# Kernel optimization log

Measured on AMD Instinct MI355X. Metric: run time of the kernel, lower is better.

Reference implementation:

```python
import jax, jax.numpy as jnp
import numpy as np

EPS_SINKHORN = 0.01   # entropic regularization (cost / eps)
EPS_LOG = 1e-8        # numerical epsilon inside logs
NUM_ITERS = 50


def setup_inputs() -> dict:
    key = jax.random.key(0)
    k1, k2 = jax.random.split(key)
    B, N = 8, 2048
    x1 = jax.random.normal(k1, (B, N, 3), dtype=jnp.float32)
    x2 = jax.random.normal(k2, (B, N, 3), dtype=jnp.float32)
    return {"x1": x1, "x2": x2}


def reference(x1, x2):
    # x1, x2: [B, N, 3] point clouds
    B, N, _ = x1.shape
    # pairwise squared-distance cost matrix: [B, N, N]
    cost = jnp.sum((x1[:, :, None, :] - x2[:, None, :, :]) ** 2, axis=-1)
    K = jnp.exp(-cost / EPS_SINKHORN)  # constant across iterations

    inv_n = jnp.float32(1.0 / N)
    mu = jnp.full((B, N), inv_n, dtype=cost.dtype)
    nu = jnp.full((B, N), inv_n, dtype=cost.dtype)
    log_mu = jnp.log(mu + EPS_LOG)
    log_nu = jnp.log(nu + EPS_LOG)

    def step(carry, _):
        u, v = carry
        # row update: sum_j K_ij * exp(v_j)
        u = log_mu - jnp.log(jnp.einsum('bij,bj->bi', K, jnp.exp(v)) + EPS_LOG)
        # col update: sum_i K_ij * exp(u_i)
        v = log_nu - jnp.log(jnp.einsum('bij,bi->bj', K, jnp.exp(u)) + EPS_LOG)
        return (u, v), None

    u0 = jnp.zeros((B, N), dtype=cost.dtype)
    v0 = jnp.zeros((B, N), dtype=cost.dtype)
    (u, v), _ = jax.lax.scan(step, (u0, v0), None, length=NUM_ITERS)

    transport = K * jnp.exp(u[:, :, None] + v[:, None, :])  # [B, N, N]
    emd = jnp.sum(transport * cost, axis=(1, 2))            # [B]
    return emd
```

## Files before the change

kernel.cpp:

```cpp
#include <hip/hip_runtime.h>
#include <cmath>

#define BATCH 8
#define NPT   2048
#define NPAIR (NPT / 2)
#define NPTS  (BATCH * NPT)
#define TILES 64
#define GRID_MAIN (BATCH * TILES)
#define THREADS 512
#define RPW   4
#define ITERS 50

#define C_LOG2E 1.4426950408889634f
#define NEG100C (-144.26950408889634f)
#define S200C   288.53900817779268f
#define EPS_LOG 1e-8f
#define LN2_01  0.006931471805599453f

typedef float v2f __attribute__((ext_vector_type(2)));
typedef float v4f __attribute__((ext_vector_type(4)));
typedef unsigned long long u64t;

static __device__ __forceinline__ float fast_exp2(float x) {
#if __has_builtin(__builtin_amdgcn_exp2f)
    return __builtin_amdgcn_exp2f(x);
#else
    return exp2f(x);
#endif
}

static __device__ __forceinline__ v2f pk_fma(v2f a, v2f b, v2f c) {
    v2f d;
    asm("v_pk_fma_f32 %0, %1, %2, %3" : "=v"(d) : "v"(a), "v"(b), "v"(c));
    return d;
}
static __device__ __forceinline__ v2f pk_add(v2f a, v2f b) {
    v2f d;
    asm("v_pk_add_f32 %0, %1, %2" : "=v"(d) : "v"(a), "v"(b));
    return d;
}

static __device__ __forceinline__ float gload(const float* p) {
    return __hip_atomic_load(p, __ATOMIC_RELAXED, __HIP_MEMORY_SCOPE_AGENT);
}
static __device__ __forceinline__ void gstore(float* p, float val) {
    __hip_atomic_store(p, val, __ATOMIC_RELAXED, __HIP_MEMORY_SCOPE_AGENT);
}
static __device__ __forceinline__ u64t gload2(const float* p) {
    return __hip_atomic_load((const u64t*)p, __ATOMIC_RELAXED,
                             __HIP_MEMORY_SCOPE_AGENT);
}

__global__ void init_kernel(float* __restrict__ out,
                            unsigned int* __restrict__ flags) {
    int t = threadIdx.x;
    if (t < BATCH) out[t] = 0.0f;
    flags[t] = 0u;
}

static __device__ __forceinline__ void flag_barrier(unsigned int* bflags,
                                                    int tile, int wave,
                                                    int lane,
                                                    unsigned int phase) {
    __syncthreads();
    if (wave == 0) {
        if (lane == 0)
            __hip_atomic_store(&bflags[tile], phase, __ATOMIC_RELAXED,
                               __HIP_MEMORY_SCOPE_AGENT);
        while (__hip_atomic_load(&bflags[lane], __ATOMIC_RELAXED,
                                 __HIP_MEMORY_SCOPE_AGENT) < phase) {
            __builtin_amdgcn_s_sleep(1);
        }
    }
    __syncthreads();
    __builtin_amdgcn_sched_barrier(0);
}

static __device__ __forceinline__ void fold_dual(v4f* cdZW, const float* dual,
        int base, int tid, const float (&Pa)[2], const float (&Pb)[2]) {
    u64t d0 = gload2(dual + base + 4 * tid);
    u64t d1 = gload2(dual + base + 4 * tid + 2);
    float a0 = __uint_as_float((unsigned)d0);
    float b0 = __uint_as_float((unsigned)(d0 >> 32));
    float a1 = __uint_as_float((unsigned)d1);
    float b1 = __uint_as_float((unsigned)(d1 >> 32));
    reinterpret_cast<v2f*>(&cdZW[2 * tid])[1] =
        (v2f){fmaf(C_LOG2E, a0, Pa[0]), fmaf(C_LOG2E, b0, Pb[0])};
    reinterpret_cast<v2f*>(&cdZW[2 * tid + 1])[1] =
        (v2f){fmaf(C_LOG2E, a1, Pa[1]), fmaf(C_LOG2E, b1, Pb[1])};
}

static __device__ __forceinline__ void half_pass(
        const v4f* cdXY, const v4f* cdZW,
        const v2f (&rx)[RPW], const v2f (&ry)[RPW],
        const v2f (&rz)[RPW], const v2f (&rc)[RPW],
        float* __restrict__ dual_out, int outbase, int lane, float log_mu)
{
    v2f acc[RPW];
#pragma unroll
    for (int r = 0; r < RPW; r++) acc[r] = (v2f){0.0f, 0.0f};

#pragma unroll 2
    for (int jp = 0; jp < NPAIR; jp += 64) {
        v4f a  = cdXY[jp + lane];
        v4f bz = cdZW[jp + lane];
        v2f xx = __builtin_shufflevector(a,  a,  0, 1);
        v2f yy = __builtin_shufflevector(a,  a,  2, 3);
        v2f zz = __builtin_shufflevector(bz, bz, 0, 1);
        v2f ww = __builtin_shufflevector(bz, bz, 2, 3);
#pragma unroll
        for (int r = 0; r < RPW; r++) {
            v2f t = pk_fma(xx, rx[r], ww);
            t = pk_fma(yy, ry[r], t);
            t = pk_fma(zz, rz[r], t);
            t = pk_add(t, rc[r]);
            acc[r].x += fast_exp2(t.x);
            acc[r].y += fast_exp2(t.y);
        }
    }

    float sel = 1.0f;
#pragma unroll
    for (int r = 0; r < RPW; r++) {
        float s = acc[r].x + acc[r].y;
#pragma unroll
        for (int m = 32; m >= 1; m >>= 1) s += __shfl_xor(s, m, 64);
        if (lane == r) sel = s;
    }
    float res = log_mu - __logf(sel + EPS_LOG);
    if (lane < RPW) gstore(&dual_out[outbase + lane], res);
}

__global__ __launch_bounds__(THREADS, 4) void sinkhorn_kernel(
        const float* __restrict__ x1, const float* __restrict__ x2,
        float* __restrict__ u, float* __restrict__ v,
        unsigned int* __restrict__ flags, float* __restrict__ out)
{
    __shared__ v4f cd1XY[NPAIR], cd1ZW[NPAIR];
    __shared__ v4f cd2XY[NPAIR], cd2ZW[NPAIR];

    const int b    = blockIdx.x / TILES;
    const int tile = blockIdx.x % TILES;
    const int base = b * NPT;
    unsigned int* bflags = flags + b * TILES;

    const int tid  = threadIdx.x;
    const int wave = tid >> 6;
    const int lane = tid & 63;
    const int row0 = tile * 32 + wave * RPW;

    const float log_mu = logf(1.0f / (float)NPT + EPS_LOG);

    float P1a[2], P1b[2], P2a[2], P2b[2];
#pragma unroll
    for (int k = 0; k < 2; k++) {
        int q = 2 * tid + k;
        const float* p = x1 + 3 * (base + 2 * q);
        float ax = p[0], ay = p[1], az = p[2];
        float bx = p[3], by = p[4], bz = p[5];
        float na = fmaf(ax, ax, fmaf(ay, ay, az * az));
        float nb = fmaf(bx, bx, fmaf(by, by, bz * bz));
        P1a[k] = na * NEG100C;  P1b[k] = nb * NEG100C;
        cd1XY[q] = (v4f){ax * S200C, bx * S200C, ay * S200C, by * S200C};
        cd1ZW[q] = (v4f){az * S200C, bz * S200C, P1a[k], P1b[k]};

        p = x2 + 3 * (base + 2 * q);
        ax = p[0]; ay = p[1]; az = p[2];
        bx = p[3]; by = p[4]; bz = p[5];
        na = fmaf(ax, ax, fmaf(ay, ay, az * az));
        nb = fmaf(bx, bx, fmaf(by, by, bz * bz));
        P2a[k] = na * NEG100C;  P2b[k] = nb * NEG100C;
        cd2XY[q] = (v4f){ax * S200C, bx * S200C, ay * S200C, by * S200C};
        cd2ZW[q] = (v4f){az * S200C, bz * S200C, P2a[k], P2b[k]};
    }

    v2f rx1[RPW], ry1[RPW], rz1[RPW], rc1[RPW];
    v2f rx2[RPW], ry2[RPW], rz2[RPW], rc2[RPW];
    float rc1s[RPW];
#pragma unroll
    for (int r = 0; r < RPW; r++) {
        const float* p = x1 + 3 * (base + row0 + r);
        float a = p[0], bb = p[1], c = p[2];
        float nn = NEG100C * fmaf(a, a, fmaf(bb, bb, c * c));
        rx1[r] = (v2f){a, a};  ry1[r] = (v2f){bb, bb};
        rz1[r] = (v2f){c, c};  rc1[r] = (v2f){nn, nn};
        rc1s[r] = nn;
        p = x2 + 3 * (base + row0 + r);
        a = p[0]; bb = p[1]; c = p[2];
        nn = NEG100C * fmaf(a, a, fmaf(bb, bb, c * c));
        rx2[r] = (v2f){a, a};  ry2[r] = (v2f){bb, bb};
        rz2[r] = (v2f){c, c};  rc2[r] = (v2f){nn, nn};
    }
    __syncthreads();

    unsigned int phase = 0;
    for (int it = 0; it < ITERS; it++) {
        if (it > 0) {
            fold_dual(cd2ZW, v, base, tid, P2a, P2b);
            __syncthreads();
        }
        half_pass(cd2XY, cd2ZW, rx1, ry1, rz1, rc1, u, base + row0, lane, log_mu);
        flag_barrier(bflags, tile, wave, lane, ++phase);

        fold_dual(cd1ZW, u, base, tid, P1a, P1b);
        __syncthreads();
        half_pass(cd1XY, cd1ZW, rx2, ry2, rz2, rc2, v, base + row0, lane, log_mu);
        flag_barrier(bflags, tile, wave, lane, ++phase);
    }

    v2f* cvp = reinterpret_cast<v2f*>(cd1XY);
    {
        u64t d0 = gload2(v + base + 4 * tid);
        u64t d1 = gload2(v + base + 4 * tid + 2);
        float a0 = __uint_as_float((unsigned)d0);
        float b0 = __uint_as_float((unsigned)(d0 >> 32));
        float a1 = __uint_as_float((unsigned)d1);
        float b1 = __uint_as_float((unsigned)(d1 >> 32));
        reinterpret_cast<v2f*>(&cd2ZW[2 * tid])[1] =
            (v2f){fmaf(C_LOG2E, a0, P2a[0]), fmaf(C_LOG2E, b0, P2b[0])};
        reinterpret_cast<v2f*>(&cd2ZW[2 * tid + 1])[1] =
            (v2f){fmaf(C_LOG2E, a1, P2a[1]), fmaf(C_LOG2E, b1, P2b[1])};
        cvp[2 * tid]     = (v2f){0.01f * a0, 0.01f * b0};
        cvp[2 * tid + 1] = (v2f){0.01f * a1, 0.01f * b1};
    }
    __syncthreads();

    v2f rcc[RPW], su[RPW];
#pragma unroll
    for (int r = 0; r < RPW; r++) {
        float ur  = gload(&u[base + row0 + r]);
        float rcs = fmaf(C_LOG2E, ur, rc1s[r]);
        rcc[r] = (v2f){rcs, rcs};
        float sus = 0.01f * ur;
        su[r] = (v2f){sus, sus};
    }

    const v2f NL2 = {-LN2_01, -LN2_01};
    v2f eacc = {0.0f, 0.0f};
#pragma unroll 2
    for (int jp = 0; jp < NPAIR; jp += 64) {
        v4f a   = cd2XY[jp + lane];
        v4f bz  = cd2ZW[jp + lane];
        v2f cv2 = cvp[jp + lane];
        v2f xx = __builtin_shufflevector(a,  a,  0, 1);
        v2f yy = __builtin_shufflevector(a,  a,  2, 3);
        v2f zz = __builtin_shufflevector(bz, bz, 0, 1);
        v2f ww = __builtin_shufflevector(bz, bz, 2, 3);
#pragma unroll
        for (int r = 0; r < RPW; r++) {
            v2f t = pk_fma(xx, rx1[r], ww);
            t = pk_fma(yy, ry1[r], t);
            t = pk_fma(zz, rz1[r], t);
            t = pk_add(t, rcc[r]);
            v2f c2 = pk_fma(t, NL2, pk_add(su[r], cv2));
            eacc.x = fmaf(fast_exp2(t.x), c2.x, eacc.x);
            eacc.y = fmaf(fast_exp2(t.y), c2.y, eacc.y);
        }
    }
    float es = eacc.x + eacc.y;
#pragma unroll
    for (int m = 32; m >= 1; m >>= 1) es += __shfl_xor(es, m, 64);

    float* wsum = reinterpret_cast<float*>(cd2XY);
    if (lane == 0) wsum[wave] = es;
    __syncthreads();
    if (tid == 0) {
        float s = 0.0f;
#pragma unroll
        for (int w = 0; w < THREADS / 64; w++) s += wsum[w];
        atomicAdd(&out[b], s);
    }
}

extern "C" void kernel_launch(void* const* d_in, const int* in_sizes, int n_in,
                              void* d_out, int out_size, void* d_ws, size_t ws_size,
                              hipStream_t stream) {
    (void)in_sizes; (void)n_in; (void)out_size; (void)ws_size;
    const float* x1 = (const float*)d_in[0];
    const float* x2 = (const float*)d_in[1];
    float* out = (float*)d_out;

    char* ws = (char*)d_ws;
    float* u = (float*)ws;
    float* v = u + NPTS;
    unsigned int* flags = (unsigned int*)(v + NPTS);

    init_kernel<<<1, 512, 0, stream>>>(out, flags);
    sinkhorn_kernel<<<GRID_MAIN, THREADS, 0, stream>>>(x1, x2, u, v, flags, out);
}
```

Baseline: 843.2 us.

## Process two batches per block with split arrive/wait barriers over 256 blocks

Each block now handles the same row tile for two batches (b and b+4) with 1024 threads and 2 rows per wave, shrinking the grid to 256 blocks. The grid barrier is split into an arrive step and a wait step, so the second batch's half-pass runs before the block waits on the first batch's flags. The dual fold is merged into the loop body and the last iteration skips the v fold. The intent is to hide barrier latency and fit the persistent grid on the available CUs, at the cost of larger LDS use per block and fewer rows per wave to amortize each shared-memory load.

```diff
diff --git a/kernel.cpp b/kernel.cpp
--- a/kernel.cpp
+++ b/kernel.cpp
@@ -6,9 +6,9 @@
 #define NPAIR (NPT / 2)
 #define NPTS  (BATCH * NPT)
 #define TILES 64
-#define GRID_MAIN (BATCH * TILES)
-#define THREADS 512
-#define RPW   4
+#define GRID_MAIN 256
+#define THREADS 1024
+#define RPW   2
 #define ITERS 50
 
 #define C_LOG2E 1.4426950408889634f
@@ -58,36 +58,24 @@
     flags[t] = 0u;
 }
 
-static __device__ __forceinline__ void flag_barrier(unsigned int* bflags,
-                                                    int tile, int wave,
-                                                    int lane,
-                                                    unsigned int phase) {
-    __syncthreads();
+static __device__ __forceinline__ void bar_arrive(unsigned int* flags,
+                                                  int slot, unsigned int ph) {
+    __syncthreads();
+    if (threadIdx.x == 0)
+        __hip_atomic_store(&flags[slot], ph, __ATOMIC_RELAXED,
+                           __HIP_MEMORY_SCOPE_AGENT);
+}
+static __device__ __forceinline__ void bar_wait(const unsigned int* bflags,
+                                                int wave, int lane,
+                                                unsigned int ph) {
     if (wave == 0) {
-        if (lane == 0)
-            __hip_atomic_store(&bflags[tile], phase, __ATOMIC_RELAXED,
-                               __HIP_MEMORY_SCOPE_AGENT);
         while (__hip_atomic_load(&bflags[lane], __ATOMIC_RELAXED,
-                                 __HIP_MEMORY_SCOPE_AGENT) < phase) {
+                                 __HIP_MEMORY_SCOPE_AGENT) < ph) {
             __builtin_amdgcn_s_sleep(1);
         }
     }
     __syncthreads();
     __builtin_amdgcn_sched_barrier(0);
-}
-
-static __device__ __forceinline__ void fold_dual(v4f* cdZW, const float* dual,
-        int base, int tid, const float (&Pa)[2], const float (&Pb)[2]) {
-    u64t d0 = gload2(dual + base + 4 * tid);
-    u64t d1 = gload2(dual + base + 4 * tid + 2);
-    float a0 = __uint_as_float((unsigned)d0);
-    float b0 = __uint_as_float((unsigned)(d0 >> 32));
-    float a1 = __uint_as_float((unsigned)d1);
-    float b1 = __uint_as_float((unsigned)(d1 >> 32));
-    reinterpret_cast<v2f*>(&cdZW[2 * tid])[1] =
-        (v2f){fmaf(C_LOG2E, a0, Pa[0]), fmaf(C_LOG2E, b0, Pb[0])};
-    reinterpret_cast<v2f*>(&cdZW[2 * tid + 1])[1] =
-        (v2f){fmaf(C_LOG2E, a1, Pa[1]), fmaf(C_LOG2E, b1, Pb[1])};
 }
 
 static __device__ __forceinline__ void half_pass(
@@ -136,13 +124,16 @@
         float* __restrict__ u, float* __restrict__ v,
         unsigned int* __restrict__ flags, float* __restrict__ out)
 {
-    __shared__ v4f cd1XY[NPAIR], cd1ZW[NPAIR];
-    __shared__ v4f cd2XY[NPAIR], cd2ZW[NPAIR];
-
-    const int b    = blockIdx.x / TILES;
+    __shared__ v4f c1XY[2][NPAIR], c1ZW[2][NPAIR];
+    __shared__ v4f c2XY[2][NPAIR], c2ZW[2][NPAIR];
+
+    const int b0   = blockIdx.x / TILES;
     const int tile = blockIdx.x % TILES;
-    const int base = b * NPT;
-    unsigned int* bflags = flags + b * TILES;
+    const int bA = b0, bB = b0 + 4;
+    const int baseA = bA * NPT, baseB = bB * NPT;
+    const int slotA = bA * TILES + tile, slotB = bB * TILES + tile;
+    const unsigned int* flA = flags + bA * TILES;
+    const unsigned int* flB = flags + bB * TILES;
 
     const int tid  = threadIdx.x;
     const int wave = tid >> 6;
@@ -153,122 +144,168 @@
 
     float P1a[2], P1b[2], P2a[2], P2b[2];
 #pragma unroll
-    for (int k = 0; k < 2; k++) {
-        int q = 2 * tid + k;
-        const float* p = x1 + 3 * (base + 2 * q);
+    for (int g = 0; g < 2; g++) {
+        int base = g ? baseB : baseA;
+        const float* p = x1 + 3 * (base + 2 * tid);
         float ax = p[0], ay = p[1], az = p[2];
         float bx = p[3], by = p[4], bz = p[5];
         float na = fmaf(ax, ax, fmaf(ay, ay, az * az));
         float nb = fmaf(bx, bx, fmaf(by, by, bz * bz));
-        P1a[k] = na * NEG100C;  P1b[k] = nb * NEG100C;
-        cd1XY[q] = (v4f){ax * S200C, bx * S200C, ay * S200C, by * S200C};
-        cd1ZW[q] = (v4f){az * S200C, bz * S200C, P1a[k], P1b[k]};
-
-        p = x2 + 3 * (base + 2 * q);
+        P1a[g] = na * NEG100C;  P1b[g] = nb * NEG100C;
+        c1XY[g][tid] = (v4f){ax * S200C, bx * S200C, ay * S200C, by * S200C};
+        c1ZW[g][tid] = (v4f){az * S200C, bz * S200C, P1a[g], P1b[g]};
+
+        p = x2 + 3 * (base + 2 * tid);
         ax = p[0]; ay = p[1]; az = p[2];
         bx = p[3]; by = p[4]; bz = p[5];
         na = fmaf(ax, ax, fmaf(ay, ay, az * az));
         nb = fmaf(bx, bx, fmaf(by, by, bz * bz));
-        P2a[k] = na * NEG100C;  P2b[k] = nb * NEG100C;
-        cd2XY[q] = (v4f){ax * S200C, bx * S200C, ay * S200C, by * S200C};
-        cd2ZW[q] = (v4f){az * S200C, bz * S200C, P2a[k], P2b[k]};
-    }
-
-    v2f rx1[RPW], ry1[RPW], rz1[RPW], rc1[RPW];
-    v2f rx2[RPW], ry2[RPW], rz2[RPW], rc2[RPW];
-    float rc1s[RPW];
-#pragma unroll
-    for (int r = 0; r < RPW; r++) {
-        const float* p = x1 + 3 * (base + row0 + r);
-        float a = p[0], bb = p[1], c = p[2];
-        float nn = NEG100C * fmaf(a, a, fmaf(bb, bb, c * c));
-        rx1[r] = (v2f){a, a};  ry1[r] = (v2f){bb, bb};
-        rz1[r] = (v2f){c, c};  rc1[r] = (v2f){nn, nn};
-        rc1s[r] = nn;
-        p = x2 + 3 * (base + row0 + r);
-        a = p[0]; bb = p[1]; c = p[2];
-        nn = NEG100C * fmaf(a, a, fmaf(bb, bb, c * c));
-        rx2[r] = (v2f){a, a};  ry2[r] = (v2f){bb, bb};
-        rz2[r] = (v2f){c, c};  rc2[r] = (v2f){nn, nn};
-    }
-    __syncthreads();
-
-    unsigned int phase = 0;
+        P2a[g] = na * NEG100C;  P2b[g] = nb * NEG100C;
+        c2XY[g][tid] = (v4f){ax * S200C, bx * S200C, ay * S200C, by * S200C};
+        c2ZW[g][tid] = (v4f){az * S200C, bz * S200C, P2a[g], P2b[g]};
+    }
+
+    v2f rx1[2][RPW], ry1[2][RPW], rz1[2][RPW], rc1[2][RPW];
+    v2f rx2[2][RPW], ry2[2][RPW], rz2[2][RPW], rc2[2][RPW];
+    float rc1s[2][RPW];
+#pragma unroll
+    for (int g = 0; g < 2; g++) {
+        int base = g ? baseB : baseA;
+#pragma unroll
+        for (int r = 0; r < RPW; r++) {
+            const float* p = x1 + 3 * (base + row0 + r);
+            float a = p[0], bb = p[1], c = p[2];
+            float nn = NEG100C * fmaf(a, a, fmaf(bb, bb, c * c));
+            rx1[g][r] = (v2f){a, a};  ry1[g][r] = (v2f){bb, bb};
+            rz1[g][r] = (v2f){c, c};  rc1[g][r] = (v2f){nn, nn};
+            rc1s[g][r] = nn;
+            p = x2 + 3 * (base + row0 + r);
+            a = p[0]; bb = p[1]; c = p[2];
+            nn = NEG100C * fmaf(a, a, fmaf(bb, bb, c * c));
+            rx2[g][r] = (v2f){a, a};  ry2[g][r] = (v2f){bb, bb};
+            rz2[g][r] = (v2f){c, c};  rc2[g][r] = (v2f){nn, nn};
+        }
+    }
+    __syncthreads();
+
+    unsigned int ph = 0;
     for (int it = 0; it < ITERS; it++) {
-        if (it > 0) {
-            fold_dual(cd2ZW, v, base, tid, P2a, P2b);
-            __syncthreads();
-        }
-        half_pass(cd2XY, cd2ZW, rx1, ry1, rz1, rc1, u, base + row0, lane, log_mu);
-        flag_barrier(bflags, tile, wave, lane, ++phase);
-
-        fold_dual(cd1ZW, u, base, tid, P1a, P1b);
+        half_pass(c2XY[0], c2ZW[0], rx1[0], ry1[0], rz1[0], rc1[0],
+                  u, baseA + row0, lane, log_mu);
+        bar_arrive(flags, slotA, ph + 1);
+        half_pass(c2XY[1], c2ZW[1], rx1[1], ry1[1], rz1[1], rc1[1],
+                  u, baseB + row0, lane, log_mu);
+        bar_arrive(flags, slotB, ph + 1);
+        bar_wait(flA, wave, lane, ph + 1);
+        bar_wait(flB, wave, lane, ph + 1);
+        {
+            u64t dA = gload2(u + baseA + 2 * tid);
+            u64t dB = gload2(u + baseB + 2 * tid);
+            float aA = __uint_as_float((unsigned)dA);
+            float bA2 = __uint_as_float((unsigned)(dA >> 32));
+            float aB = __uint_as_float((unsigned)dB);
+            float bB2 = __uint_as_float((unsigned)(dB >> 32));
+            reinterpret_cast<v2f*>(&c1ZW[0][tid])[1] =
+                (v2f){fmaf(C_LOG2E, aA, P1a[0]), fmaf(C_LOG2E, bA2, P1b[0])};
+            reinterpret_cast<v2f*>(&c1ZW[1][tid])[1] =
+                (v2f){fmaf(C_LOG2E, aB, P1a[1]), fmaf(C_LOG2E, bB2, P1b[1])};
+        }
         __syncthreads();
-        half_pass(cd1XY, cd1ZW, rx2, ry2, rz2, rc2, v, base + row0, lane, log_mu);
-        flag_barrier(bflags, tile, wave, lane, ++phase);
-    }
-
-    v2f* cvp = reinterpret_cast<v2f*>(cd1XY);
+
+        half_pass(c1XY[0], c1ZW[0], rx2[0], ry2[0], rz2[0], rc2[0],
+                  v, baseA + row0, lane, log_mu);
+        bar_arrive(flags, slotA, ph + 2);
+        half_pass(c1XY[1], c1ZW[1], rx2[1], ry2[1], rz2[1], rc2[1],
+                  v, baseB + row0, lane, log_mu);
+        bar_arrive(flags, slotB, ph + 2);
+        bar_wait(flA, wave, lane, ph + 2);
+        bar_wait(flB, wave, lane, ph + 2);
+        if (it < ITERS - 1) {
+            u64t dA = gload2(v + baseA + 2 * tid);
+            u64t dB = gload2(v + baseB + 2 * tid);
+            float aA = __uint_as_float((unsigned)dA);
+            float bA2 = __uint_as_float((unsigned)(dA >> 32));
+            float aB = __uint_as_float((unsigned)dB);
+            float bB2 = __uint_as_float((unsigned)(dB >> 32));
+            reinterpret_cast<v2f*>(&c2ZW[0][tid])[1] =
+                (v2f){fmaf(C_LOG2E, aA, P2a[0]), fmaf(C_LOG2E, bA2, P2b[0])};
+            reinterpret_cast<v2f*>(&c2ZW[1][tid])[1] =
+                (v2f){fmaf(C_LOG2E, aB, P2a[1]), fmaf(C_LOG2E, bB2, P2b[1])};
+        }
+        __syncthreads();
+        ph += 2;
+    }
+
+    v2f* cvp0 = reinterpret_cast<v2f*>(c1XY[0]);
+    v2f* cvp1 = reinterpret_cast<v2f*>(c1XY[1]);
     {
-        u64t d0 = gload2(v + base + 4 * tid);
-        u64t d1 = gload2(v + base + 4 * tid + 2);
-        float a0 = __uint_as_float((unsigned)d0);
-        float b0 = __uint_as_float((unsigned)(d0 >> 32));
-        float a1 = __uint_as_float((unsigned)d1);
-        float b1 = __uint_as_float((unsigned)(d1 >> 32));
-        reinterpret_cast<v2f*>(&cd2ZW[2 * tid])[1] =
-            (v2f){fmaf(C_LOG2E, a0, P2a[0]), fmaf(C_LOG2E, b0, P2b[0])};
-        reinterpret_cast<v2f*>(&cd2ZW[2 * tid + 1])[1] =
-            (v2f){fmaf(C_LOG2E, a1, P2a[1]), fmaf(C_LOG2E, b1, P2b[1])};
-        cvp[2 * tid]     = (v2f){0.01f * a0, 0.01f * b0};
-        cvp[2 * tid + 1] = (v2f){0.01f * a1, 0.01f * b1};
-    }
-    __syncthreads();
-
-    v2f rcc[RPW], su[RPW];
-#pragma unroll
-    for (int r = 0; r < RPW; r++) {
-        float ur  = gload(&u[base + row0 + r]);
-        float rcs = fmaf(C_LOG2E, ur, rc1s[r]);
-        rcc[r] = (v2f){rcs, rcs};
-        float sus = 0.01f * ur;
-        su[r] = (v2f){sus, sus};
-    }
+        u64t dA = gload2(v + baseA + 2 * tid);
+        u64t dB = gload2(v + baseB + 2 * tid);
+        float aA = __uint_as_float((unsigned)dA);
+        float bA2 = __uint_as_float((unsigned)(dA >> 32));
+        float aB = __uint_as_float((unsigned)dB);
+        float bB2 = __uint_as_float((unsigned)(dB >> 32));
+        reinterpret_cast<v2f*>(&c2ZW[0][tid])[1] =
+            (v2f){fmaf(C_LOG2E, aA, P2a[0]), fmaf(C_LOG2E, bA2, P2b[0])};
+        reinterpret_cast<v2f*>(&c2ZW[1][tid])[1] =
+            (v2f){fmaf(C_LOG2E, aB, P2a[1]), fmaf(C_LOG2E, bB2, P2b[1])};
+        cvp0[tid] = (v2f){0.01f * aA, 0.01f * bA2};
+        cvp1[tid] = (v2f){0.01f * aB, 0.01f * bB2};
+    }
+    __syncthreads();
 
     const v2f NL2 = {-LN2_01, -LN2_01};
-    v2f eacc = {0.0f, 0.0f};
+    float es[2];
+#pragma unroll
+    for (int g = 0; g < 2; g++) {
+        int base = g ? baseB : baseA;
+        v2f* cvp = g ? cvp1 : cvp0;
+        v2f rcc[RPW], su[RPW];
+#pragma unroll
+        for (int r = 0; r < RPW; r++) {
+            float ur  = gload(&u[base + row0 + r]);
+            float rcs = fmaf(C_LOG2E, ur, rc1s[g][r]);
+            rcc[r] = (v2f){rcs, rcs};
+            float sus = 0.01f * ur;
+            su[r] = (v2f){sus, sus};
+        }
+        v2f eacc = {0.0f, 0.0f};
 #pragma unroll 2
-    for (int jp = 0; jp < NPAIR; jp += 64) {
-        v4f a   = cd2XY[jp + lane];
-        v4f bz  = cd2ZW[jp + lane];
-        v2f cv2 = cvp[jp + lane];
-        v2f xx = __builtin_shufflevector(a,  a,  0, 1);
-        v2f yy = __builtin_shufflevector(a,  a,  2, 3);
-        v2f zz = __builtin_shufflevector(bz, bz, 0, 1);
-        v2f ww = __builtin_shufflevector(bz, bz, 2, 3);
-#pragma unroll
-        for (int r = 0; r < RPW; r++) {
-            v2f t = pk_fma(xx, rx1[r], ww);
-            t = pk_fma(yy, ry1[r], t);
-            t = pk_fma(zz, rz1[r], t);
-            t = pk_add(t, rcc[r]);
-            v2f c2 = pk_fma(t, NL2, pk_add(su[r], cv2));
-            eacc.x = fmaf(fast_exp2(t.x), c2.x, eacc.x);
-            eacc.y = fmaf(fast_exp2(t.y), c2.y, eacc.y);
-        }
-    }
-    float es = eacc.x + eacc.y;
-#pragma unroll
-    for (int m = 32; m >= 1; m >>= 1) es += __shfl_xor(es, m, 64);
-
-    float* wsum = reinterpret_cast<float*>(cd2XY);
-    if (lane == 0) wsum[wave] = es;
+        for (int jp = 0; jp < NPAIR; jp += 64) {
+            v4f a   = c2XY[g][jp + lane];
+            v4f bz  = c2ZW[g][jp + lane];
+            v2f cv2 = cvp[jp + lane];
+            v2f xx = __builtin_shufflevector(a,  a,  0, 1);
+            v2f yy = __builtin_shufflevector(a,  a,  2, 3);
+            v2f zz = __builtin_shufflevector(bz, bz, 0, 1);
+            v2f ww = __builtin_shufflevector(bz, bz, 2, 3);
+#pragma unroll
+            for (int r = 0; r < RPW; r++) {
+                v2f t = pk_fma(xx, rx1[g][r], ww);
+                t = pk_fma(yy, ry1[g][r], t);
+                t = pk_fma(zz, rz1[g][r], t);
+                t = pk_add(t, rcc[r]);
+                v2f c2 = pk_fma(t, NL2, pk_add(su[r], cv2));
+                eacc.x = fmaf(fast_exp2(t.x), c2.x, eacc.x);
+                eacc.y = fmaf(fast_exp2(t.y), c2.y, eacc.y);
+            }
+        }
+        float e = eacc.x + eacc.y;
+#pragma unroll
+        for (int m = 32; m >= 1; m >>= 1) e += __shfl_xor(e, m, 64);
+        es[g] = e;
+    }
+
+    float* wsumA = reinterpret_cast<float*>(c1ZW[0]);
+    float* wsumB = reinterpret_cast<float*>(c1ZW[1]);
+    if (lane == 0) { wsumA[wave] = es[0]; wsumB[wave] = es[1]; }
     __syncthreads();
     if (tid == 0) {
-        float s = 0.0f;
-#pragma unroll
-        for (int w = 0; w < THREADS / 64; w++) s += wsum[w];
-        atomicAdd(&out[b], s);
+        float sA = 0.0f, sB = 0.0f;
+#pragma unroll
+        for (int w = 0; w < THREADS / 64; w++) { sA += wsumA[w]; sB += wsumB[w]; }
+        atomicAdd(&out[bA], sA);
+        atomicAdd(&out[bB], sB);
     }
 }
 
```

After: 850.6 us. No clear change (+0.9%).

## Remap Sinkhorn passes to one row per lane with cross-wave LDS reduction

Applied to the files above, without the earlier changes.

Changes the work split. Before, each wave owned 4 rows and its lanes strided over columns. Now each lane owns one row and walks a contiguous 64-pair column chunk, so all lanes in a half-wave read the same LDS address (broadcast). Row sums are combined with one xor-shuffle and then a shared-memory partial array summed across the 8 waves, replacing the per-row 6-step wave reductions. In exchange it adds a block barrier per half-pass, issues more LDS loads per exponential, and loses reuse of each column load across several rows.

```diff
diff --git a/kernel.cpp b/kernel.cpp
--- a/kernel.cpp
+++ b/kernel.cpp
@@ -8,7 +8,6 @@
 #define TILES 64
 #define GRID_MAIN (BATCH * TILES)
 #define THREADS 512
-#define RPW   4
 #define ITERS 50
 
 #define C_LOG2E 1.4426950408889634f
@@ -90,45 +89,27 @@
         (v2f){fmaf(C_LOG2E, a1, Pa[1]), fmaf(C_LOG2E, b1, Pb[1])};
 }
 
-static __device__ __forceinline__ void half_pass(
-        const v4f* cdXY, const v4f* cdZW,
-        const v2f (&rx)[RPW], const v2f (&ry)[RPW],
-        const v2f (&rz)[RPW], const v2f (&rc)[RPW],
-        float* __restrict__ dual_out, int outbase, int lane, float log_mu)
+static __device__ __forceinline__ float half_core(
+        const v4f* cdXY, const v4f* cdZW, int p0,
+        v2f RX, v2f RY, v2f RZ, v2f RC)
 {
-    v2f acc[RPW];
-#pragma unroll
-    for (int r = 0; r < RPW; r++) acc[r] = (v2f){0.0f, 0.0f};
-
-#pragma unroll 2
-    for (int jp = 0; jp < NPAIR; jp += 64) {
-        v4f a  = cdXY[jp + lane];
-        v4f bz = cdZW[jp + lane];
+    float accx = 0.0f, accy = 0.0f;
+#pragma unroll 4
+    for (int s = 0; s < 64; s++) {
+        v4f a  = cdXY[p0 + s];
+        v4f bz = cdZW[p0 + s];
         v2f xx = __builtin_shufflevector(a,  a,  0, 1);
         v2f yy = __builtin_shufflevector(a,  a,  2, 3);
         v2f zz = __builtin_shufflevector(bz, bz, 0, 1);
         v2f ww = __builtin_shufflevector(bz, bz, 2, 3);
-#pragma unroll
-        for (int r = 0; r < RPW; r++) {
-            v2f t = pk_fma(xx, rx[r], ww);
-            t = pk_fma(yy, ry[r], t);
-            t = pk_fma(zz, rz[r], t);
-            t = pk_add(t, rc[r]);
-            acc[r].x += fast_exp2(t.x);
-            acc[r].y += fast_exp2(t.y);
-        }
-    }
-
-    float sel = 1.0f;
-#pragma unroll
-    for (int r = 0; r < RPW; r++) {
-        float s = acc[r].x + acc[r].y;
-#pragma unroll
-        for (int m = 32; m >= 1; m >>= 1) s += __shfl_xor(s, m, 64);
-        if (lane == r) sel = s;
-    }
-    float res = log_mu - __logf(sel + EPS_LOG);
-    if (lane < RPW) gstore(&dual_out[outbase + lane], res);
+        v2f t = pk_fma(xx, RX, ww);
+        t = pk_fma(yy, RY, t);
+        t = pk_fma(zz, RZ, t);
+        t = pk_add(t, RC);
+        accx += fast_exp2(t.x);
+        accy += fast_exp2(t.y);
+    }
+    return accx + accy;
 }
 
 __global__ __launch_bounds__(THREADS, 4) void sinkhorn_kernel(
@@ -138,6 +119,7 @@
 {
     __shared__ v4f cd1XY[NPAIR], cd1ZW[NPAIR];
     __shared__ v4f cd2XY[NPAIR], cd2ZW[NPAIR];
+    __shared__ float part[32][9];
 
     const int b    = blockIdx.x / TILES;
     const int tile = blockIdx.x % TILES;
@@ -147,7 +129,10 @@
     const int tid  = threadIdx.x;
     const int wave = tid >> 6;
     const int lane = tid & 63;
-    const int row0 = tile * 32 + wave * RPW;
+    const int rloc = lane & 31;
+    const int ch   = lane >> 5;
+    const int row  = tile * 32 + rloc;
+    const int p0   = wave * 128 + ch * 64;
 
     const float log_mu = logf(1.0f / (float)NPT + EPS_LOG);
 
@@ -174,38 +159,60 @@
         cd2ZW[q] = (v4f){az * S200C, bz * S200C, P2a[k], P2b[k]};
     }
 
-    v2f rx1[RPW], ry1[RPW], rz1[RPW], rc1[RPW];
-    v2f rx2[RPW], ry2[RPW], rz2[RPW], rc2[RPW];
-    float rc1s[RPW];
-#pragma unroll
-    for (int r = 0; r < RPW; r++) {
-        const float* p = x1 + 3 * (base + row0 + r);
+    v2f RX1, RY1, RZ1, RC1, RX2, RY2, RZ2, RC2;
+    float rc1s;
+    {
+        const float* p = x1 + 3 * (base + row);
         float a = p[0], bb = p[1], c = p[2];
         float nn = NEG100C * fmaf(a, a, fmaf(bb, bb, c * c));
-        rx1[r] = (v2f){a, a};  ry1[r] = (v2f){bb, bb};
-        rz1[r] = (v2f){c, c};  rc1[r] = (v2f){nn, nn};
-        rc1s[r] = nn;
-        p = x2 + 3 * (base + row0 + r);
+        RX1 = (v2f){a, a};  RY1 = (v2f){bb, bb};
+        RZ1 = (v2f){c, c};  RC1 = (v2f){nn, nn};
+        rc1s = nn;
+        p = x2 + 3 * (base + row);
         a = p[0]; bb = p[1]; c = p[2];
         nn = NEG100C * fmaf(a, a, fmaf(bb, bb, c * c));
-        rx2[r] = (v2f){a, a};  ry2[r] = (v2f){bb, bb};
-        rz2[r] = (v2f){c, c};  rc2[r] = (v2f){nn, nn};
-    }
-    __syncthreads();
-
-    unsigned int phase = 0;
+        RX2 = (v2f){a, a};  RY2 = (v2f){bb, bb};
+        RZ2 = (v2f){c, c};  RC2 = (v2f){nn, nn};
+    }
+    __syncthreads();
+
+    unsigned int ph = 0;
     for (int it = 0; it < ITERS; it++) {
         if (it > 0) {
             fold_dual(cd2ZW, v, base, tid, P2a, P2b);
             __syncthreads();
         }
-        half_pass(cd2XY, cd2ZW, rx1, ry1, rz1, rc1, u, base + row0, lane, log_mu);
-        flag_barrier(bflags, tile, wave, lane, ++phase);
+        {
+            float s = half_core(cd2XY, cd2ZW, p0, RX1, RY1, RZ1, RC1);
+            s += __shfl_xor(s, 32, 64);
+            if (lane < 32) part[rloc][wave] = s;
+            __syncthreads();
+            if (wave == 0) {
+                float t = 0.0f;
+#pragma unroll
+                for (int w = 0; w < 8; w++) t += part[rloc][w];
+                float res = log_mu - __logf(t + EPS_LOG);
+                if (lane < 32) gstore(&u[base + row], res);
+            }
+        }
+        flag_barrier(bflags, tile, wave, lane, ++ph);
 
         fold_dual(cd1ZW, u, base, tid, P1a, P1b);
         __syncthreads();
-        half_pass(cd1XY, cd1ZW, rx2, ry2, rz2, rc2, v, base + row0, lane, log_mu);
-        flag_barrier(bflags, tile, wave, lane, ++phase);
+        {
+            float s = half_core(cd1XY, cd1ZW, p0, RX2, RY2, RZ2, RC2);
+            s += __shfl_xor(s, 32, 64);
+            if (lane < 32) part[rloc][wave] = s;
+            __syncthreads();
+            if (wave == 0) {
+                float t = 0.0f;
+#pragma unroll
+                for (int w = 0; w < 8; w++) t += part[rloc][w];
+                float res = log_mu - __logf(t + EPS_LOG);
+                if (lane < 32) gstore(&v[base + row], res);
+            }
+        }
+        flag_barrier(bflags, tile, wave, lane, ++ph);
     }
 
     v2f* cvp = reinterpret_cast<v2f*>(cd1XY);
@@ -225,49 +232,42 @@
     }
     __syncthreads();
 
-    v2f rcc[RPW], su[RPW];
-#pragma unroll
-    for (int r = 0; r < RPW; r++) {
-        float ur  = gload(&u[base + row0 + r]);
-        float rcs = fmaf(C_LOG2E, ur, rc1s[r]);
-        rcc[r] = (v2f){rcs, rcs};
-        float sus = 0.01f * ur;
-        su[r] = (v2f){sus, sus};
-    }
+    float ur = gload(&u[base + row]);
+    float rcs = fmaf(C_LOG2E, ur, rc1s);
+    v2f RCC = (v2f){rcs, rcs};
+    float sus = 0.01f * ur;
+    v2f SU = (v2f){sus, sus};
 
     const v2f NL2 = {-LN2_01, -LN2_01};
     v2f eacc = {0.0f, 0.0f};
-#pragma unroll 2
-    for (int jp = 0; jp < NPAIR; jp += 64) {
-        v4f a   = cd2XY[jp + lane];
-        v4f bz  = cd2ZW[jp + lane];
-        v2f cv2 = cvp[jp + lane];
+#pragma unroll 4
+    for (int s = 0; s < 64; s++) {
+        v4f a   = cd2XY[p0 + s];
+        v4f bz  = cd2ZW[p0 + s];
+        v2f cv2 = cvp[p0 + s];
         v2f xx = __builtin_shufflevector(a,  a,  0, 1);
         v2f yy = __builtin_shufflevector(a,  a,  2, 3);
         v2f zz = __builtin_shufflevector(bz, bz, 0, 1);
         v2f ww = __builtin_shufflevector(bz, bz, 2, 3);
-#pragma unroll
-        for (int r = 0; r < RPW; r++) {
-            v2f t = pk_fma(xx, rx1[r], ww);
-            t = pk_fma(yy, ry1[r], t);
-            t = pk_fma(zz, rz1[r], t);
-            t = pk_add(t, rcc[r]);
-            v2f c2 = pk_fma(t, NL2, pk_add(su[r], cv2));
-            eacc.x = fmaf(fast_exp2(t.x), c2.x, eacc.x);
-            eacc.y = fmaf(fast_exp2(t.y), c2.y, eacc.y);
-        }
+        v2f t = pk_fma(xx, RX1, ww);
+        t = pk_fma(yy, RY1, t);
+        t = pk_fma(zz, RZ1, t);
+        t = pk_add(t, RCC);
+        v2f c2 = pk_fma(t, NL2, pk_add(SU, cv2));
+        eacc.x = fmaf(fast_exp2(t.x), c2.x, eacc.x);
+        eacc.y = fmaf(fast_exp2(t.y), c2.y, eacc.y);
     }
     float es = eacc.x + eacc.y;
 #pragma unroll
     for (int m = 32; m >= 1; m >>= 1) es += __shfl_xor(es, m, 64);
 
-    float* wsum = reinterpret_cast<float*>(cd2XY);
-    if (lane == 0) wsum[wave] = es;
+    __syncthreads();
+    if (lane == 0) part[0][wave] = es;
     __syncthreads();
     if (tid == 0) {
         float s = 0.0f;
 #pragma unroll
-        for (int w = 0; w < THREADS / 64; w++) s += wsum[w];
+        for (int w = 0; w < 8; w++) s += part[0][w];
         atomicAdd(&out[b], s);
     }
 }
```

Result: faster. 813.7 us (-3.5%).
